# Optimization experiments

Hardware: AMD Instinct MI355X
Metric: run time of the kernel (lower is better)

Reference implementation:

```python
import jax, jax.numpy as jnp
import numpy as np

D = 128
H = 4
L = 3
MAX_LEN = 696


def _pe(max_len, d):
    pos = jnp.arange(max_len, dtype=jnp.float32)[:, None]
    div = jnp.exp(jnp.arange(0, d, 2, dtype=jnp.float32) * (-jnp.log(jnp.float32(10000.0)) / d))
    pe = jnp.zeros((max_len, d), dtype=jnp.float32)
    pe = pe.at[:, 0::2].set(jnp.sin(pos * div))
    pe = pe.at[:, 1::2].set(jnp.cos(pos * div))
    return pe  # [max_len, d]


def _ln(x, w, b, eps=1e-5):
    m = jnp.mean(x, axis=-1, keepdims=True)
    v = jnp.mean((x - m) ** 2, axis=-1, keepdims=True)
    return (x - m) / jnp.sqrt(v + eps) * w + b


def _mha(xq, xkv, wqkv, bqkv, wo, bo, mask=None):
    # xq: [Tq,B,d], xkv: [Tk,B,d] (seq-first, torch convention)
    d = xq.shape[-1]
    hd = d // H
    q = xq @ wqkv[:d].T + bqkv[:d]
    k = xkv @ wqkv[d:2 * d].T + bqkv[d:2 * d]
    v = xkv @ wqkv[2 * d:].T + bqkv[2 * d:]

    def split(t):
        T, B, _ = t.shape
        return t.reshape(T, B, H, hd).transpose(1, 2, 0, 3)  # [B,H,T,hd]

    qh, kh, vh = split(q), split(k), split(v)
    s = jnp.einsum('bhqd,bhkd->bhqk', qh, kh) / jnp.sqrt(jnp.float32(hd))
    if mask is not None:
        s = jnp.where(mask, jnp.float32(-1e9), s)
    a = jax.nn.softmax(s, axis=-1)
    o = jnp.einsum('bhqk,bhkd->bhqd', a, vh)
    Tq, B = xq.shape[0], xq.shape[1]
    o = o.transpose(2, 0, 1, 3).reshape(Tq, B, d)
    return o @ wo.T + bo


def _forward(src, tgt, emb_in_w, emb_in_b, emb_out_w, emb_out_b,
             enc_qkv_w, enc_qkv_b, enc_proj_w, enc_proj_b,
             enc_ff1_w, enc_ff1_b, enc_ff2_w, enc_ff2_b, enc_ln_w, enc_ln_b,
             dec_sa_qkv_w, dec_sa_qkv_b, dec_sa_proj_w, dec_sa_proj_b,
             dec_ca_qkv_w, dec_ca_qkv_b, dec_ca_proj_w, dec_ca_proj_b,
             dec_ff1_w, dec_ff1_b, dec_ff2_w, dec_ff2_b, dec_ln_w, dec_ln_b,
             head_w, head_b):
    pe = _pe(MAX_LEN, D)
    # ---- encoder ----
    src_p = jnp.transpose(src, (2, 0, 1))  # [S,B,1]
    x = src_p @ emb_in_w.T + emb_in_b + pe[:src_p.shape[0], None, :]
    for i in range(L):
        a = _mha(x, x, enc_qkv_w[i], enc_qkv_b[i], enc_proj_w[i], enc_proj_b[i])
        x = _ln(x + a, enc_ln_w[i, 0], enc_ln_b[i, 0])
        f = jax.nn.relu(x @ enc_ff1_w[i].T + enc_ff1_b[i]) @ enc_ff2_w[i].T + enc_ff2_b[i]
        x = _ln(x + f, enc_ln_w[i, 1], enc_ln_b[i, 1])
    memory = x  # [S,B,D]
    # ---- decoder (full teacher forcing: loop collapses to one causal pass) ----
    tgt_p = jnp.transpose(tgt, (2, 0, 1))  # [T,B,1]
    T = tgt_p.shape[0]
    y = tgt_p[:T - 1] @ emb_out_w.T + emb_out_b  # [T-1,B,D]
    # original code applies pos encoding only to the initial token of the decode loop
    y = y.at[0].add(pe[0])
    mask = jnp.triu(jnp.ones((T - 1, T - 1), dtype=bool), k=1)  # True = masked
    for i in range(L):
        a = _mha(y, y, dec_sa_qkv_w[i], dec_sa_qkv_b[i], dec_sa_proj_w[i], dec_sa_proj_b[i], mask=mask)
        y = _ln(y + a, dec_ln_w[i, 0], dec_ln_b[i, 0])
        c = _mha(y, memory, dec_ca_qkv_w[i], dec_ca_qkv_b[i], dec_ca_proj_w[i], dec_ca_proj_b[i])
        y = _ln(y + c, dec_ln_w[i, 1], dec_ln_b[i, 1])
        f = jax.nn.relu(y @ dec_ff1_w[i].T + dec_ff1_b[i]) @ dec_ff2_w[i].T + dec_ff2_b[i]
        y = _ln(y + f, dec_ln_w[i, 2], dec_ln_b[i, 2])
    out = y @ head_w.T + head_b  # [T-1,B,1]
    return jnp.transpose(out, (1, 2, 0))  # [B,1,T-1]


def setup_inputs() -> dict:
    key = jax.random.key(0)
    ks = iter(jax.random.split(key, 64))

    def n(shape, s=0.02):
        return (jax.random.normal(next(ks), shape) * s).astype(jnp.float32)

    return {
        'src': jax.random.normal(next(ks), (64, 1, 696), dtype=jnp.float32),
        'tgt': jax.random.normal(next(ks), (64, 1, 512), dtype=jnp.float32),
        'emb_in_w': n((D, 1)), 'emb_in_b': n((D,)),
        'emb_out_w': n((D, 1)), 'emb_out_b': n((D,)),
        'enc_qkv_w': n((L, 3 * D, D)), 'enc_qkv_b': n((L, 3 * D)),
        'enc_proj_w': n((L, D, D)), 'enc_proj_b': n((L, D)),
        'enc_ff1_w': n((L, D, D)), 'enc_ff1_b': n((L, D)),
        'enc_ff2_w': n((L, D, D)), 'enc_ff2_b': n((L, D)),
        'enc_ln_w': jnp.ones((L, 2, D), dtype=jnp.float32),
        'enc_ln_b': jnp.zeros((L, 2, D), dtype=jnp.float32),
        'dec_sa_qkv_w': n((L, 3 * D, D)), 'dec_sa_qkv_b': n((L, 3 * D)),
        'dec_sa_proj_w': n((L, D, D)), 'dec_sa_proj_b': n((L, D)),
        'dec_ca_qkv_w': n((L, 3 * D, D)), 'dec_ca_qkv_b': n((L, 3 * D)),
        'dec_ca_proj_w': n((L, D, D)), 'dec_ca_proj_b': n((L, D)),
        'dec_ff1_w': n((L, D, D)), 'dec_ff1_b': n((L, D)),
        'dec_ff2_w': n((L, D, D)), 'dec_ff2_b': n((L, D)),
        'dec_ln_w': jnp.ones((L, 3, D), dtype=jnp.float32),
        'dec_ln_b': jnp.zeros((L, 3, D), dtype=jnp.float32),
        'head_w': n((1, D)), 'head_b': n((1,)),
    }


def reference(src, tgt, emb_in_w, emb_in_b, emb_out_w, emb_out_b,
              enc_qkv_w, enc_qkv_b, enc_proj_w, enc_proj_b,
              enc_ff1_w, enc_ff1_b, enc_ff2_w, enc_ff2_b, enc_ln_w, enc_ln_b,
              dec_sa_qkv_w, dec_sa_qkv_b, dec_sa_proj_w, dec_sa_proj_b,
              dec_ca_qkv_w, dec_ca_qkv_b, dec_ca_proj_w, dec_ca_proj_b,
              dec_ff1_w, dec_ff1_b, dec_ff2_w, dec_ff2_b, dec_ln_w, dec_ln_b,
              head_w, head_b):
    return _forward(src, tgt, emb_in_w, emb_in_b, emb_out_w, emb_out_b,
                    enc_qkv_w, enc_qkv_b, enc_proj_w, enc_proj_b,
                    enc_ff1_w, enc_ff1_b, enc_ff2_w, enc_ff2_b, enc_ln_w, enc_ln_b,
                    dec_sa_qkv_w, dec_sa_qkv_b, dec_sa_proj_w, dec_sa_proj_b,
                    dec_ca_qkv_w, dec_ca_qkv_b, dec_ca_proj_w, dec_ca_proj_b,
                    dec_ff1_w, dec_ff1_b, dec_ff2_w, dec_ff2_b, dec_ln_w, dec_ln_b,
                    head_w, head_b)
```

## Files before the change

### kernel.cpp

```cpp
#include <hip/hip_runtime.h>
#include <hip/hip_bf16.h>


typedef unsigned short u16;
typedef unsigned int u32;
typedef float f32x4 __attribute__((ext_vector_type(4)));
typedef float f32x2 __attribute__((ext_vector_type(2)));
typedef float f32x16 __attribute__((ext_vector_type(16)));
typedef unsigned short u16x8 __attribute__((ext_vector_type(8)));
typedef unsigned int u32x2 __attribute__((ext_vector_type(2)));
typedef unsigned int u32x4 __attribute__((ext_vector_type(4)));
typedef __bf16 bf16x8 __attribute__((ext_vector_type(8)));

static __device__ __forceinline__ float bf2f(u16 u) {
  u32 x = ((u32)u) << 16;
  return __builtin_bit_cast(float, x);
}
static __device__ __forceinline__ u16 f2bf(float f) {
  u32 x = __builtin_bit_cast(u32, f);
  u32 r = (x + 0x7fffu + ((x >> 16) & 1u)) >> 16;
  return (u16)r;
}
static __device__ __forceinline__ f32x4 mfma16(bf16x8 a, bf16x8 b, f32x4 c) {
  return __builtin_amdgcn_mfma_f32_16x16x32_bf16(a, b, c, 0, 0, 0);
}
static __device__ __forceinline__ f32x16 mfma32(bf16x8 a, bf16x8 b, f32x16 c) {
  return __builtin_amdgcn_mfma_f32_32x32x16_bf16(a, b, c, 0, 0, 0);
}
static __device__ __forceinline__ void plswap(u32& a, u32& b) {
  u32x2 r = __builtin_amdgcn_permlane32_swap(a, b, false, false);
  a = r.x; b = r.y;
}

__global__ void detect_k(const u32* __restrict__ ones, int* __restrict__ flag) {
  *flag = (ones[0] == 0x3F803F80u) ? 1 : 0;
}

struct CvtArgs {
  const void* p[32];
  int n[32];
  int off[32];
};

__global__ __launch_bounds__(256) void cvt_all(CvtArgs A, const int* __restrict__ flag,
                                               float* __restrict__ poolf,
                                               u16* __restrict__ poolb) {
  int ti = blockIdx.y;
  int i = blockIdx.x * 256 + threadIdx.x;
  int n = A.n[ti];
  if (i >= n) return;
  int o = A.off[ti] + i;
  if (*flag) {
    u16 raw = ((const u16*)A.p[ti])[i];
    poolb[o] = raw;
    poolf[o] = bf2f(raw);
  } else {
    float v = ((const float*)A.p[ti])[i];
    poolf[o] = v;
    poolb[o] = f2bf(v);
  }
}

__global__ void embed_enc(const float* __restrict__ src, const float* __restrict__ w,
                          const float* __restrict__ b, float* __restrict__ X,
                          u16* __restrict__ Xb) {
  int s = blockIdx.x, d = threadIdx.x;
  float freq = __expf(-(float)(d & 126) * 0.07195578415606394f);
  float arg = (float)s * freq;
  float pe = (d & 1) ? cosf(arg) : sinf(arg);
  float wd = w[d], bd = b[d];
  for (int bb = 0; bb < 64; ++bb) {
    float v = src[bb * 696 + s] * wd + bd + pe;
    size_t o = ((size_t)s * 64 + bb) * 128 + d;
    X[o] = v;
    Xb[o] = f2bf(v);
  }
}

__global__ void embed_dec(const float* __restrict__ tgt, const float* __restrict__ w,
                          const float* __restrict__ b, float* __restrict__ Y,
                          u16* __restrict__ Yb) {
  int tt = blockIdx.x, d = threadIdx.x;
  float wd = w[d], bd = b[d];
  float pe0 = (tt == 0 && (d & 1)) ? 1.0f : 0.0f;
  for (int bb = 0; bb < 64; ++bb) {
    float v = tgt[bb * 512 + tt] * wd + bd + pe0;
    size_t o = ((size_t)tt * 64 + bb) * 128 + d;
    Y[o] = v;
    Yb[o] = f2bf(v);
  }
}

__global__ __launch_bounds__(256) void gemm_lnq(
    const u16* __restrict__ Ab, const u16* __restrict__ Wp, const float* __restrict__ bp,
    float* __restrict__ R, const float* __restrict__ ln1w, const float* __restrict__ ln1b,
    const u16* __restrict__ Wq, const float* __restrict__ bq, u16* __restrict__ Qg) {
  __shared__ u16 WBUF[128][136];
  __shared__ u16 XBUF[64][136];
  const int t = threadIdx.x;
  const int n0 = blockIdx.x << 6;
  const int wv = t >> 6, lane = t & 63, lg = lane >> 4, lr = lane & 15;
  const int r0 = n0 + (wv << 4);
  const float QS = 0.17677669529663687f * 1.4426950408889634f;

#pragma unroll
  for (int i = 0; i < 8; ++i) {
    int idx = t + (i << 8);
    int r = idx >> 4, c = (idx & 15) << 3;
    *(u16x8*)&WBUF[r][c] = *(const u16x8*)(Wp + ((size_t)r << 7) + c);
  }
  bf16x8 afr[4];
#pragma unroll
  for (int ks = 0; ks < 4; ++ks)
    afr[ks] = *(const bf16x8*)(Ab + ((size_t)(r0 + lr) << 7) + (ks << 5) + (lg << 3));
  __syncthreads();

  f32x4 acc[8] = {};
#pragma unroll
  for (int ks = 0; ks < 4; ++ks) {
#pragma unroll
    for (int cb = 0; cb < 8; ++cb) {
      bf16x8 bfr = *(const bf16x8*)&WBUF[(cb << 4) + lr][(ks << 5) + (lg << 3)];
      acc[cb] = mfma16(afr[ks], bfr, acc[cb]);
    }
  }
  float x1[8][4];
#pragma unroll
  for (int cb = 0; cb < 8; ++cb) {
    float bv = bp[(cb << 4) + lr];
#pragma unroll
    for (int r = 0; r < 4; ++r) {
      size_t row = (size_t)(r0 + (lg << 2) + r);
      x1[cb][r] = acc[cb][r] + bv + R[(row << 7) + (cb << 4) + lr];
    }
  }
#pragma unroll
  for (int r = 0; r < 4; ++r) {
    float s = 0.0f, s2 = 0.0f;
#pragma unroll
    for (int cb = 0; cb < 8; ++cb) { float v = x1[cb][r]; s += v; s2 += v * v; }
    s += __shfl_xor(s, 1); s2 += __shfl_xor(s2, 1);
    s += __shfl_xor(s, 2); s2 += __shfl_xor(s2, 2);
    s += __shfl_xor(s, 4); s2 += __shfl_xor(s2, 4);
    s += __shfl_xor(s, 8); s2 += __shfl_xor(s2, 8);
    float m = s * 0.0078125f;
    float rstd = rsqrtf(s2 * 0.0078125f - m * m + 1e-5f);
#pragma unroll
    for (int cb = 0; cb < 8; ++cb)
      x1[cb][r] = (x1[cb][r] - m) * rstd * ln1w[(cb << 4) + lr] + ln1b[(cb << 4) + lr];
  }
#pragma unroll
  for (int cb = 0; cb < 8; ++cb)
#pragma unroll
    for (int r = 0; r < 4; ++r) {
      size_t o = ((size_t)(r0 + (lg << 2) + r) << 7) + (cb << 4) + lr;
      R[o] = x1[cb][r];
      XBUF[(wv << 4) + (lg << 2) + r][(cb << 4) + lr] = f2bf(x1[cb][r]);
    }
  __syncthreads();

#pragma unroll
  for (int i = 0; i < 8; ++i) {
    int idx = t + (i << 8);
    int r = idx >> 4, c = (idx & 15) << 3;
    *(u16x8*)&WBUF[r][c] = *(const u16x8*)(Wq + ((size_t)r << 7) + c);
  }
#pragma unroll
  for (int ks = 0; ks < 4; ++ks)
    afr[ks] = *(const bf16x8*)&XBUF[(wv << 4) + lr][(ks << 5) + (lg << 3)];
  __syncthreads();

#pragma unroll
  for (int cb = 0; cb < 8; ++cb) acc[cb] = f32x4{0, 0, 0, 0};
#pragma unroll
  for (int ks = 0; ks < 4; ++ks) {
#pragma unroll
    for (int cb = 0; cb < 8; ++cb) {
      bf16x8 bfr = *(const bf16x8*)&WBUF[(cb << 4) + lr][(ks << 5) + (lg << 3)];
      acc[cb] = mfma16(afr[ks], bfr, acc[cb]);
    }
  }
#pragma unroll
  for (int cb = 0; cb < 8; ++cb) {
    float bv = bq[(cb << 4) + lr];
#pragma unroll
    for (int r = 0; r < 4; ++r) {
      size_t o = ((size_t)(r0 + (lg << 2) + r) << 7) + (cb << 4) + lr;
      Qg[o] = f2bf((acc[cb][r] + bv) * QS);
    }
  }
}

__global__ __launch_bounds__(256) void gemm_plff(
    const u16* __restrict__ Ab, const u16* __restrict__ Wp, const float* __restrict__ bp,
    const u16* __restrict__ W1, const float* __restrict__ b1,
    const u16* __restrict__ W2, const float* __restrict__ b2,
    float* __restrict__ R, u16* __restrict__ Rb,
    const float* __restrict__ ln1w, const float* __restrict__ ln1b,
    const float* __restrict__ ln2w, const float* __restrict__ ln2b) {
  __shared__ u16 WBUF[128][136];
  __shared__ u16 XBUF[64][136];
  const int t = threadIdx.x;
  const int n0 = blockIdx.x << 6;
  const int wv = t >> 6, lane = t & 63, lg = lane >> 4, lr = lane & 15;
  const int r0 = n0 + (wv << 4);

#pragma unroll
  for (int i = 0; i < 8; ++i) {
    int idx = t + (i << 8);
    int r = idx >> 4, c = (idx & 15) << 3;
    *(u16x8*)&WBUF[r][c] = *(const u16x8*)(Wp + ((size_t)r << 7) + c);
  }
  bf16x8 afr[4];
#pragma unroll
  for (int ks = 0; ks < 4; ++ks)
    afr[ks] = *(const bf16x8*)(Ab + ((size_t)(r0 + lr) << 7) + (ks << 5) + (lg << 3));
  __syncthreads();

  f32x4 acc[8] = {};
#pragma unroll
  for (int ks = 0; ks < 4; ++ks) {
#pragma unroll
    for (int cb = 0; cb < 8; ++cb) {
      bf16x8 bfr = *(const bf16x8*)&WBUF[(cb << 4) + lr][(ks << 5) + (lg << 3)];
      acc[cb] = mfma16(afr[ks], bfr, acc[cb]);
    }
  }
  float x1[8][4];
#pragma unroll
  for (int cb = 0; cb < 8; ++cb) {
    float bv = bp[(cb << 4) + lr];
#pragma unroll
    for (int r = 0; r < 4; ++r) {
      size_t row = (size_t)(r0 + (lg << 2) + r);
      x1[cb][r] = acc[cb][r] + bv + R[(row << 7) + (cb << 4) + lr];
    }
  }
#pragma unroll
  for (int r = 0; r < 4; ++r) {
    float s = 0.0f, s2 = 0.0f;
#pragma unroll
    for (int cb = 0; cb < 8; ++cb) { float v = x1[cb][r]; s += v; s2 += v * v; }
    s += __shfl_xor(s, 1); s2 += __shfl_xor(s2, 1);
    s += __shfl_xor(s, 2); s2 += __shfl_xor(s2, 2);
    s += __shfl_xor(s, 4); s2 += __shfl_xor(s2, 4);
    s += __shfl_xor(s, 8); s2 += __shfl_xor(s2, 8);
    float m = s * 0.0078125f;
    float rstd = rsqrtf(s2 * 0.0078125f - m * m + 1e-5f);
#pragma unroll
    for (int cb = 0; cb < 8; ++cb)
      x1[cb][r] = (x1[cb][r] - m) * rstd * ln1w[(cb << 4) + lr] + ln1b[(cb << 4) + lr];
  }
#pragma unroll
  for (int cb = 0; cb < 8; ++cb)
#pragma unroll
    for (int r = 0; r < 4; ++r)
      XBUF[(wv << 4) + (lg << 2) + r][(cb << 4) + lr] = f2bf(x1[cb][r]);
  __syncthreads();

#pragma unroll
  for (int i = 0; i < 8; ++i) {
    int idx = t + (i << 8);
    int r = idx >> 4, c = (idx & 15) << 3;
    *(u16x8*)&WBUF[r][c] = *(const u16x8*)(W1 + ((size_t)r << 7) + c);
  }
#pragma unroll
  for (int ks = 0; ks < 4; ++ks)
    afr[ks] = *(const bf16x8*)&XBUF[(wv << 4) + lr][(ks << 5) + (lg << 3)];
  __syncthreads();

#pragma unroll
  for (int cb = 0; cb < 8; ++cb) acc[cb] = f32x4{0, 0, 0, 0};
#pragma unroll
  for (int ks = 0; ks < 4; ++ks) {
#pragma unroll
    for (int cb = 0; cb < 8; ++cb) {
      bf16x8 bfr = *(const bf16x8*)&WBUF[(cb << 4) + lr][(ks << 5) + (lg << 3)];
      acc[cb] = mfma16(afr[ks], bfr, acc[cb]);
    }
  }
  float h[8][4];
#pragma unroll
  for (int cb = 0; cb < 8; ++cb) {
    float bv = b1[(cb << 4) + lr];
#pragma unroll
    for (int r = 0; r < 4; ++r) h[cb][r] = fmaxf(acc[cb][r] + bv, 0.0f);
  }
  __syncthreads();

#pragma unroll
  for (int cb = 0; cb < 8; ++cb)
#pragma unroll
    for (int r = 0; r < 4; ++r)
      XBUF[(wv << 4) + (lg << 2) + r][(cb << 4) + lr] = f2bf(h[cb][r]);
#pragma unroll
  for (int i = 0; i < 8; ++i) {
    int idx = t + (i << 8);
    int r = idx >> 4, c = (idx & 15) << 3;
    *(u16x8*)&WBUF[r][c] = *(const u16x8*)(W2 + ((size_t)r << 7) + c);
  }
  __syncthreads();

#pragma unroll
  for (int ks = 0; ks < 4; ++ks)
    afr[ks] = *(const bf16x8*)&XBUF[(wv << 4) + lr][(ks << 5) + (lg << 3)];
#pragma unroll
  for (int cb = 0; cb < 8; ++cb) acc[cb] = f32x4{0, 0, 0, 0};
#pragma unroll
  for (int ks = 0; ks < 4; ++ks) {
#pragma unroll
    for (int cb = 0; cb < 8; ++cb) {
      bf16x8 bfr = *(const bf16x8*)&WBUF[(cb << 4) + lr][(ks << 5) + (lg << 3)];
      acc[cb] = mfma16(afr[ks], bfr, acc[cb]);
    }
  }
  float vals[8][4];
#pragma unroll
  for (int cb = 0; cb < 8; ++cb) {
    float bv = b2[(cb << 4) + lr];
#pragma unroll
    for (int r = 0; r < 4; ++r) vals[cb][r] = acc[cb][r] + bv + x1[cb][r];
  }
#pragma unroll
  for (int r = 0; r < 4; ++r) {
    float s = 0.0f, s2 = 0.0f;
#pragma unroll
    for (int cb = 0; cb < 8; ++cb) { float v = vals[cb][r]; s += v; s2 += v * v; }
    s += __shfl_xor(s, 1); s2 += __shfl_xor(s2, 1);
    s += __shfl_xor(s, 2); s2 += __shfl_xor(s2, 2);
    s += __shfl_xor(s, 4); s2 += __shfl_xor(s2, 4);
    s += __shfl_xor(s, 8); s2 += __shfl_xor(s2, 8);
    float m = s * 0.0078125f;
    float rstd = rsqrtf(s2 * 0.0078125f - m * m + 1e-5f);
#pragma unroll
    for (int cb = 0; cb < 8; ++cb) {
      float v = (vals[cb][r] - m) * rstd * ln2w[(cb << 4) + lr] + ln2b[(cb << 4) + lr];
      size_t o = ((size_t)(r0 + (lg << 2) + r) << 7) + (cb << 4) + lr;
      R[o] = v;
      Rb[o] = f2bf(v);
    }
  }
}

__global__ __launch_bounds__(256) void gemm_qkv(
    const u16* __restrict__ Xb, const u16* __restrict__ Wb,
    const float* __restrict__ bias, u16* __restrict__ Qg,
    u16* __restrict__ Kg, u16* __restrict__ Vg, int M, int kbase, int vbase) {
  __shared__ u16 Xs[64][136];
  __shared__ u16 Ws[64][136];
  const int t = threadIdx.x;
  const int n0 = blockIdx.x << 6, m0 = blockIdx.y << 6;
  const int wq = t >> 6, lane = t & 63, lg = lane >> 4, lr = lane & 15;
  const int wr = (wq >> 1) << 5, wc = (wq & 1) << 5;
  const float QS = 0.17677669529663687f * 1.4426950408889634f;

#pragma unroll
  for (int i = 0; i < 4; ++i) {
    int idx = t + (i << 8);
    int r = idx >> 4, c = (idx & 15) << 3;
    *(u16x8*)&Xs[r][c] = *(const u16x8*)(Xb + (size_t)(n0 + r) * 128 + c);
    *(u16x8*)&Ws[r][c] = *(const u16x8*)(Wb + (size_t)(m0 + r) * 128 + c);
  }
  __syncthreads();

  f32x4 acc00 = {0,0,0,0}, acc01 = {0,0,0,0}, acc10 = {0,0,0,0}, acc11 = {0,0,0,0};
#pragma unroll
  for (int ks = 0; ks < 4; ++ks) {
    bf16x8 a0 = *(const bf16x8*)&Xs[wr + lr][(ks << 5) + (lg << 3)];
    bf16x8 a1 = *(const bf16x8*)&Xs[wr + 16 + lr][(ks << 5) + (lg << 3)];
    bf16x8 b0 = *(const bf16x8*)&Ws[wc + lr][(ks << 5) + (lg << 3)];
    bf16x8 b1 = *(const bf16x8*)&Ws[wc + 16 + lr][(ks << 5) + (lg << 3)];
    acc00 = mfma16(a0, b0, acc00);
    acc01 = mfma16(a0, b1, acc01);
    acc10 = mfma16(a1, b0, acc10);
    acc11 = mfma16(a1, b1, acc11);
  }

  f32x4 accs[2][2] = {{acc00, acc01}, {acc10, acc11}};
#pragma unroll
  for (int mi = 0; mi < 2; ++mi) {
#pragma unroll
    for (int ni = 0; ni < 2; ++ni) {
      int col = m0 + wc + (ni << 4) + lr;
      float bv = bias[col];
#pragma unroll
      for (int r = 0; r < 4; ++r) {
        int row = n0 + wr + (mi << 4) + (lg << 2) + r;
        float v = accs[mi][ni][r] + bv;
        size_t ro = (size_t)row << 7;
        if (col < kbase) {
          Qg[ro + col] = f2bf(v * QS);
        } else if (col < vbase) {
          Kg[ro + (col - kbase)] = f2bf(v);
        } else {
          Vg[ro + (col - vbase)] = f2bf(v);
        }
      }
    }
  }
}

__global__ __launch_bounds__(256) void attn_g(
    const u16* __restrict__ Qg, const u16* __restrict__ Kg,
    const u16* __restrict__ Vg, u16* __restrict__ Ob,
    int Tq, int Tk, int causal, int bpb) {
  __shared__ u16 Ks[64][44];
  __shared__ u16 Vs[32][74];
  __shared__ float Lw[4][36];
  const int t = threadIdx.x;
  const int wv = t >> 6, lane = t & 63;
  const int lq = lane & 31, hi = lane >> 5;
  const int p = blockIdx.x;
  const int idx = p >> 3;
  const int bh = ((p & 7) << 5) + idx / bpb;
  const int blk = idx % bpb;
  const int nstrips = (Tq + 31) >> 5;
  const int strip = blk * 4 + wv;
  const bool active = strip < nstrips;
  const int b = bh >> 2, h = bh & 3;
  const int qw = (active ? strip : (nstrips - 1)) << 5;

  bf16x8 qf[2];
  {
    int ql = qw + lq; if (ql > Tq - 1) ql = Tq - 1;
    const u16* qp = Qg + (((size_t)ql * 64 + b) << 7) + h * 32 + (hi << 3);
    qf[0] = *(const bf16x8*)qp;
    qf[1] = *(const bf16x8*)(qp + 16);
  }

  f32x16 o = {};
  float lsum = 0.0f;

  const int nfull = causal ? (qw >> 6) : (Tk >> 6);
  int lastcol = causal ? qw + 31 : Tk - 1;
  if (lastcol > Tk - 1) lastcol = Tk - 1;
  int ntiles = (lastcol >> 6) + 1;
  if (!active) ntiles = 0;

  int lastq_blk = blk * 128 + 127;
  if (lastq_blk > Tq - 1) lastq_blk = Tq - 1;
  int lastcol_blk = causal ? lastq_blk : Tk - 1;
  if (lastcol_blk > Tk - 1) lastcol_blk = Tk - 1;
  const int ntb = (lastcol_blk >> 6) + 1;

  const int stok = t >> 2, sc = (t & 3) << 3;

  for (int kt = 0; kt < ntb; ++kt) {
    const int k0 = kt << 6;
    __syncthreads();
    {
      int tok = k0 + stok; if (tok > Tk - 1) tok = Tk - 1;
      size_t roff = (((size_t)tok * 64 + b) << 7) + h * 32 + sc;
      *(u16x8*)&Ks[stok][sc] = *(const u16x8*)(Kg + roff);
      u16x8 vv = *(const u16x8*)(Vg + roff);
#pragma unroll
      for (int e = 0; e < 8; ++e) Vs[sc + e][stok] = vv[e];
    }
    __syncthreads();
    if (kt >= ntiles) continue;
    const bool masked = (kt >= nfull);

#pragma unroll
    for (int kb = 0; kb < 2; ++kb) {
      const int krow = (kb << 5) + lq;
      bf16x8 ka0 = *(const bf16x8*)&Ks[krow][hi << 3];
      bf16x8 ka1 = *(const bf16x8*)&Ks[krow][16 + (hi << 3)];
      f32x16 s = {};
      __builtin_amdgcn_s_setprio(1);
      s = mfma32(ka0, qf[0], s);
      s = mfma32(ka1, qf[1], s);
      __builtin_amdgcn_s_setprio(0);

      float pv[16];
#pragma unroll
      for (int r = 0; r < 16; ++r) {
        float sv = s[r];
        if (masked) {
          int kk = k0 + (kb << 5) + (r & 3) + ((r >> 2) << 3) + (hi << 2);
          int q = qw + lq;
          bool ok = causal ? (kk <= q) : (kk < Tk);
          sv = ok ? sv : -1e30f;
        }
        float e = exp2f(sv);
        pv[r] = e;
        lsum += e;
      }
      u32 u[8];
#pragma unroll
      for (int m = 0; m < 8; ++m)
        asm("v_cvt_pk_bf16_f32 %0, %1, %2" : "=v"(u[m]) : "v"(pv[2 * m]), "v"(pv[2 * m + 1]));

#pragma unroll
      for (int c = 0; c < 2; ++c) {
        u32 a0 = u[4 * c + 0], b0 = u[4 * c + 2];
        u32 a1 = u[4 * c + 1], b1 = u[4 * c + 3];
        plswap(a0, b0);
        plswap(a1, b1);
        u32x4 wv4 = {a0, a1, b0, b1};
        bf16x8 pf = __builtin_bit_cast(bf16x8, wv4);
        bf16x8 vf = *(const bf16x8*)&Vs[lq][(kb << 5) + (c << 4) + (hi << 3)];
        __builtin_amdgcn_s_setprio(1);
        o = mfma32(pf, vf, o);
        __builtin_amdgcn_s_setprio(0);
      }
    }
  }

  if (active) {
    float lt = lsum + __shfl_xor(lsum, 32);
    if (hi == 0) Lw[wv][lq] = 1.0f / lt;
    f32x4 li[4];
#pragma unroll
    for (int g = 0; g < 4; ++g)
      li[g] = *(const f32x4*)&Lw[wv][(hi << 2) + (g << 3)];
#pragma unroll
    for (int r = 0; r < 16; ++r) {
      int q = qw + (r & 3) + ((r >> 2) << 3) + (hi << 2);
      if (q < Tq) {
        Ob[(((size_t)q * 64 + b) << 7) + h * 32 + lq] = f2bf(o[r] * li[r >> 2][r & 3]);
      }
    }
  }
}

__global__ __launch_bounds__(256) void head_k(
    const float* __restrict__ Y, const float* __restrict__ w,
    const float* __restrict__ bh, void* __restrict__ out, const int* __restrict__ flag) {
  int n = (blockIdx.x << 2) + (threadIdx.x >> 6);
  int lane = threadIdx.x & 63;
  const float* yp = Y + (size_t)n * 128 + (lane << 1);
  float s = yp[0] * w[lane << 1] + yp[1] * w[(lane << 1) + 1];
#pragma unroll
  for (int off = 1; off < 64; off <<= 1) s += __shfl_xor(s, off);
  if (lane == 0) {
    int tt = n >> 6, bb = n & 63;
    float r = s + bh[0];
    int idx = bb * 511 + tt;
    if (*flag) ((u16*)out)[idx] = f2bf(r);
    else       ((float*)out)[idx] = r;
  }
}

extern "C" void kernel_launch(void* const* d_in, const int* in_sizes, int n_in,
                              void* d_out, int out_size, void* d_ws, size_t ws_size,
                              hipStream_t stream) {
  (void)out_size; (void)ws_size;
  CvtArgs A;
  long off[33]; off[0] = 0;
  int maxn = 0;
  for (int i = 0; i < 32; ++i) {
    int n = (i < n_in) ? in_sizes[i] : 0;
    A.p[i] = (i < n_in) ? d_in[i] : d_in[0];
    A.n[i] = n;
    A.off[i] = (int)off[i];
    off[i + 1] = off[i] + n;
    if (n > maxn) maxn = n;
  }
  const size_t offA = (size_t)((off[32] + 15) & ~15l);

  const size_t NE = 44544;
  const size_t ND = 32704;
  float* ws   = (float*)d_ws;
  int*   flag = (int*)d_ws;
  float* Wp   = ws + 16;
  float* Xe   = Wp + offA;
  float* Yd   = Xe + NE * 128;
  u16*   U    = (u16*)(Yd + ND * 128);
  u16*   Wb   = U;
  u16*   Xebf = Wb + offA;
  u16*   Ydbf = Xebf + NE * 128;
  u16*   TMPbf= Ydbf + ND * 128;
  u16*   Qgb  = TMPbf + NE * 128;
  u16*   Kgb  = Qgb + NE * 128;
  u16*   Vgb  = Kgb + NE * 128;

  const float* F = Wp;
  detect_k<<<1, 1, 0, stream>>>((const u32*)d_in[14], flag);
  cvt_all<<<dim3((maxn + 255) / 256, 32), 256, 0, stream>>>(A, flag, Wp, Wb);

  embed_enc<<<dim3(696), dim3(128), 0, stream>>>(F + A.off[0], F + A.off[2], F + A.off[3], Xe, Xebf);
  for (int i = 0; i < 3; ++i) {
    gemm_qkv<<<dim3(696, 6), 256, 0, stream>>>(Xebf, Wb + A.off[6] + i * 49152, F + A.off[7] + i * 384,
                                               Qgb, Kgb, Vgb, 384, 128, 256);
    attn_g<<<dim3(1536), 256, 0, stream>>>(Qgb, Kgb, Vgb, TMPbf, 696, 696, 0, 6);
    gemm_plff<<<dim3(696), 256, 0, stream>>>(TMPbf, Wb + A.off[8] + i * 16384, F + A.off[9] + i * 128,
                                             Wb + A.off[10] + i * 16384, F + A.off[11] + i * 128,
                                             Wb + A.off[12] + i * 16384, F + A.off[13] + i * 128,
                                             Xe, Xebf,
                                             F + A.off[14] + (i * 2 + 0) * 128, F + A.off[15] + (i * 2 + 0) * 128,
                                             F + A.off[14] + (i * 2 + 1) * 128, F + A.off[15] + (i * 2 + 1) * 128);
  }

  embed_dec<<<dim3(511), dim3(128), 0, stream>>>(F + A.off[1], F + A.off[4], F + A.off[5], Yd, Ydbf);
  for (int i = 0; i < 3; ++i) {
    gemm_qkv<<<dim3(511, 6), 256, 0, stream>>>(Ydbf, Wb + A.off[16] + i * 49152, F + A.off[17] + i * 384,
                                               Qgb, Kgb, Vgb, 384, 128, 256);
    attn_g<<<dim3(1024), 256, 0, stream>>>(Qgb, Kgb, Vgb, TMPbf, 511, 511, 1, 4);
    gemm_lnq<<<dim3(511), 256, 0, stream>>>(TMPbf, Wb + A.off[18] + i * 16384, F + A.off[19] + i * 128,
                                            Yd, F + A.off[28] + (i * 3 + 0) * 128, F + A.off[29] + (i * 3 + 0) * 128,
                                            Wb + A.off[20] + i * 49152, F + A.off[21] + i * 384, Qgb);
    gemm_qkv<<<dim3(696, 4), 256, 0, stream>>>(Xebf, Wb + A.off[20] + i * 49152 + 16384, F + A.off[21] + i * 384 + 128,
                                               nullptr, Kgb, Vgb, 256, 0, 128);
    attn_g<<<dim3(1024), 256, 0, stream>>>(Qgb, Kgb, Vgb, TMPbf, 511, 696, 0, 4);
    gemm_plff<<<dim3(511), 256, 0, stream>>>(TMPbf, Wb + A.off[22] + i * 16384, F + A.off[23] + i * 128,
                                             Wb + A.off[24] + i * 16384, F + A.off[25] + i * 128,
                                             Wb + A.off[26] + i * 16384, F + A.off[27] + i * 128,
                                             Yd, Ydbf,
                                             F + A.off[28] + (i * 3 + 1) * 128, F + A.off[29] + (i * 3 + 1) * 128,
                                             F + A.off[28] + (i * 3 + 2) * 128, F + A.off[29] + (i * 3 + 2) * 128);
  }

  head_k<<<dim3(8176), 256, 0, stream>>>(Yd, F + A.off[30], F + A.off[31], d_out, flag);
}
```

Before: 726.7 us.

## Double-buffer K/V tiles in attention kernel with register prefetch

The attention kernel now keeps two LDS buffers for the K and V tiles. It issues the global loads for the next tile into registers before computing on the current one, then writes them into the alternate buffer afterwards. This removes one __syncthreads per iteration and hides global load latency behind the MFMA and exp work. The cost is twice the LDS footprint and extra registers held across the compute loop, which may reduce occupancy.

```diff
diff --git a/kernel.cpp b/kernel.cpp
--- a/kernel.cpp
+++ b/kernel.cpp
@@ -404,8 +404,8 @@
     const u16* __restrict__ Qg, const u16* __restrict__ Kg,
     const u16* __restrict__ Vg, u16* __restrict__ Ob,
     int Tq, int Tk, int causal, int bpb) {
-  __shared__ u16 Ks[64][44];
-  __shared__ u16 Vs[32][74];
+  __shared__ u16 Ks[2][64][44];
+  __shared__ u16 Vs[2][32][74];
   __shared__ float Lw[4][36];
   const int t = threadIdx.x;
   const int wv = t >> 6, lane = t & 63;
@@ -445,65 +445,82 @@
 
   const int stok = t >> 2, sc = (t & 3) << 3;
 
+  u16x8 rk, rv;
+  {
+    int tok = stok; if (tok > Tk - 1) tok = Tk - 1;
+    size_t roff = (((size_t)tok * 64 + b) << 7) + h * 32 + sc;
+    rk = *(const u16x8*)(Kg + roff);
+    rv = *(const u16x8*)(Vg + roff);
+  }
+  *(u16x8*)&Ks[0][stok][sc] = rk;
+#pragma unroll
+  for (int e = 0; e < 8; ++e) Vs[0][sc + e][stok] = rv[e];
+  int cur = 0;
+
   for (int kt = 0; kt < ntb; ++kt) {
     const int k0 = kt << 6;
+    if (kt + 1 < ntb) {
+      int tok = k0 + 64 + stok; if (tok > Tk - 1) tok = Tk - 1;
+      size_t roff = (((size_t)tok * 64 + b) << 7) + h * 32 + sc;
+      rk = *(const u16x8*)(Kg + roff);
+      rv = *(const u16x8*)(Vg + roff);
+    }
     __syncthreads();
-    {
-      int tok = k0 + stok; if (tok > Tk - 1) tok = Tk - 1;
-      size_t roff = (((size_t)tok * 64 + b) << 7) + h * 32 + sc;
-      *(u16x8*)&Ks[stok][sc] = *(const u16x8*)(Kg + roff);
-      u16x8 vv = *(const u16x8*)(Vg + roff);
-#pragma unroll
-      for (int e = 0; e < 8; ++e) Vs[sc + e][stok] = vv[e];
-    }
-    __syncthreads();
-    if (kt >= ntiles) continue;
-    const bool masked = (kt >= nfull);
-
-#pragma unroll
-    for (int kb = 0; kb < 2; ++kb) {
-      const int krow = (kb << 5) + lq;
-      bf16x8 ka0 = *(const bf16x8*)&Ks[krow][hi << 3];
-      bf16x8 ka1 = *(const bf16x8*)&Ks[krow][16 + (hi << 3)];
-      f32x16 s = {};
-      __builtin_amdgcn_s_setprio(1);
-      s = mfma32(ka0, qf[0], s);
-      s = mfma32(ka1, qf[1], s);
-      __builtin_amdgcn_s_setprio(0);
-
-      float pv[16];
-#pragma unroll
-      for (int r = 0; r < 16; ++r) {
-        float sv = s[r];
-        if (masked) {
-          int kk = k0 + (kb << 5) + (r & 3) + ((r >> 2) << 3) + (hi << 2);
-          int q = qw + lq;
-          bool ok = causal ? (kk <= q) : (kk < Tk);
-          sv = ok ? sv : -1e30f;
+
+    if (kt < ntiles) {
+      const bool masked = (kt >= nfull);
+#pragma unroll
+      for (int kb = 0; kb < 2; ++kb) {
+        const int krow = (kb << 5) + lq;
+        bf16x8 ka0 = *(const bf16x8*)&Ks[cur][krow][hi << 3];
+        bf16x8 ka1 = *(const bf16x8*)&Ks[cur][krow][16 + (hi << 3)];
+        f32x16 s = {};
+        __builtin_amdgcn_s_setprio(1);
+        s = mfma32(ka0, qf[0], s);
+        s = mfma32(ka1, qf[1], s);
+        __builtin_amdgcn_s_setprio(0);
+
+        float pv[16];
+#pragma unroll
+        for (int r = 0; r < 16; ++r) {
+          float sv = s[r];
+          if (masked) {
+            int kk = k0 + (kb << 5) + (r & 3) + ((r >> 2) << 3) + (hi << 2);
+            int q = qw + lq;
+            bool ok = causal ? (kk <= q) : (kk < Tk);
+            sv = ok ? sv : -1e30f;
+          }
+          float e = exp2f(sv);
+          pv[r] = e;
+          lsum += e;
         }
-        float e = exp2f(sv);
-        pv[r] = e;
-        lsum += e;
+        u32 u[8];
+#pragma unroll
+        for (int m = 0; m < 8; ++m)
+          asm("v_cvt_pk_bf16_f32 %0, %1, %2" : "=v"(u[m]) : "v"(pv[2 * m]), "v"(pv[2 * m + 1]));
+
+#pragma unroll
+        for (int c = 0; c < 2; ++c) {
+          u32 a0 = u[4 * c + 0], b0 = u[4 * c + 2];
+          u32 a1 = u[4 * c + 1], b1 = u[4 * c + 3];
+          plswap(a0, b0);
+          plswap(a1, b1);
+          u32x4 wv4 = {a0, a1, b0, b1};
+          bf16x8 pf = __builtin_bit_cast(bf16x8, wv4);
+          bf16x8 vf = *(const bf16x8*)&Vs[cur][lq][(kb << 5) + (c << 4) + (hi << 3)];
+          __builtin_amdgcn_s_setprio(1);
+          o = mfma32(pf, vf, o);
+          __builtin_amdgcn_s_setprio(0);
+        }
       }
-      u32 u[8];
-#pragma unroll
-      for (int m = 0; m < 8; ++m)
-        asm("v_cvt_pk_bf16_f32 %0, %1, %2" : "=v"(u[m]) : "v"(pv[2 * m]), "v"(pv[2 * m + 1]));
-
-#pragma unroll
-      for (int c = 0; c < 2; ++c) {
-        u32 a0 = u[4 * c + 0], b0 = u[4 * c + 2];
-        u32 a1 = u[4 * c + 1], b1 = u[4 * c + 3];
-        plswap(a0, b0);
-        plswap(a1, b1);
-        u32x4 wv4 = {a0, a1, b0, b1};
-        bf16x8 pf = __builtin_bit_cast(bf16x8, wv4);
-        bf16x8 vf = *(const bf16x8*)&Vs[lq][(kb << 5) + (c << 4) + (hi << 3)];
-        __builtin_amdgcn_s_setprio(1);
-        o = mfma32(pf, vf, o);
-        __builtin_amdgcn_s_setprio(0);
-      }
-    }
+    }
+
+    if (kt + 1 < ntb) {
+      *(u16x8*)&Ks[cur ^ 1][stok][sc] = rk;
+#pragma unroll
+      for (int e = 0; e < 8; ++e) Vs[cur ^ 1][sc + e][stok] = rv[e];
+    }
+    cur ^= 1;
   }
 
   if (active) {
```

After: 723.9 us. No clear change (-0.4%).
